# Kernel tuning notes

Hardware: AMD Instinct MI355X
Metric: run time of the kernel (lower is better)

The kernel has to match this reference:

```python
import jax, jax.numpy as jnp
import numpy as np

N_NODES = 100000
N_EDGES = 3200000
IN_CH = 16
HIDDEN = 32
NUM_HH = 1000


def setup_inputs() -> dict:
    key = jax.random.key(0)
    ks = jax.random.split(key, 10)
    x = jax.random.normal(ks[0], (N_NODES, IN_CH), dtype=jnp.float32)
    edge_index = jax.random.randint(ks[1], (2, N_EDGES), 0, N_NODES, dtype=jnp.int64)
    s = 1.0 / np.sqrt(IN_CH)
    w1_l = jax.random.uniform(ks[2], (IN_CH, HIDDEN), jnp.float32, -s, s)
    w1_r = jax.random.uniform(ks[3], (IN_CH, HIDDEN), jnp.float32, -s, s)
    b1 = jnp.zeros((HIDDEN,), jnp.float32)
    s2 = 1.0 / np.sqrt(HIDDEN)
    w2_l = jax.random.uniform(ks[4], (HIDDEN, HIDDEN), jnp.float32, -s2, s2)
    w2_r = jax.random.uniform(ks[5], (HIDDEN, HIDDEN), jnp.float32, -s2, s2)
    b2 = jnp.zeros((HIDDEN,), jnp.float32)
    fc_w = jax.random.uniform(ks[6], (HIDDEN, NUM_HH), jnp.float32, -s2, s2)
    fc_b = jnp.zeros((NUM_HH,), jnp.float32)
    return {"x": x, "edge_index": edge_index, "w1_l": w1_l, "w1_r": w1_r, "b1": b1,
            "w2_l": w2_l, "w2_r": w2_r, "b2": b2, "fc_w": fc_w, "fc_b": fc_b}


def _sage_conv(h, src, dst, w_l, w_r, b, n_nodes):
    # mean-aggregate source features onto targets (PyG SAGEConv, aggr='mean')
    msg = h[src]                                            # [E, F] gather
    agg = jax.ops.segment_sum(msg, dst, num_segments=n_nodes)
    cnt = jax.ops.segment_sum(jnp.ones((src.shape[0], 1), h.dtype), dst,
                              num_segments=n_nodes)
    mean = agg / jnp.maximum(cnt, 1.0)
    # out = lin_l(mean_neighbors) + lin_r(x); bias lives in lin_l
    return mean @ w_l + b + h @ w_r


def reference(x, edge_index, w1_l, w1_r, b1, w2_l, w2_r, b2, fc_w, fc_b):
    src, dst = edge_index[0], edge_index[1]
    n = x.shape[0]
    h = jax.nn.relu(_sage_conv(x, src, dst, w1_l, w1_r, b1, n))
    h = jax.nn.relu(_sage_conv(h, src, dst, w2_l, w2_r, b2, n))
    return h @ fc_w + fc_b
```

## Files before the change

### kernel.cpp

```cpp
#include <hip/hip_runtime.h>

#define N_NODES 100000
#define IN_CH 16
#define HIDDEN 32
#define NUM_HH 1000

#define NPB 128
#define NBUCK ((N_NODES + NPB - 1) / NPB)
#define NCHUNK 512
#define CAP 4480

__global__ __launch_bounds__(256) void passAB(
    const int* __restrict__ src, const int* __restrict__ dst,
    int* __restrict__ gcur, unsigned* __restrict__ packed, int n_edges,
    int cepb) {
  __shared__ int hist[NBUCK];
  __shared__ int rbase[NBUCK];
  __shared__ int cur[NBUCK];
  const int tid = threadIdx.x;
  for (int i = tid; i < NBUCK; i += 256) {
    hist[i] = 0;
    cur[i] = 0;
  }
  __syncthreads();

  const int s = blockIdx.x * cepb;
  const int e = min(n_edges, s + cepb);
  for (int i = s + tid; i < e; i += 256) atomicAdd(&hist[dst[i] >> 7], 1);
  __syncthreads();

  for (int b = tid; b < NBUCK; b += 256) {
    const int h = hist[b];
    rbase[b] = h ? atomicAdd(&gcur[b], h) : 0;
  }
  __syncthreads();

  for (int i = s + tid; i < e; i += 256) {
    const int d = dst[i];
    const int b = d >> 7;
    const int off = atomicAdd(&cur[b], 1);
    const int pos = rbase[b] + off;
    if (pos < CAP)
      packed[(size_t)b * CAP + pos] =
          (unsigned)src[i] | ((unsigned)(d & (NPB - 1)) << 17);
  }
}

__global__ __launch_bounds__(512) void bucket_sort(
    unsigned* __restrict__ packed, const int* __restrict__ gcur,
    int* __restrict__ row_ptr) {
  __shared__ unsigned stage[CAP];
  __shared__ int bins[NPB];
  __shared__ int scn[NPB];
  __shared__ int cur[NPB];
  const int b = blockIdx.x;
  const int base = b * CAP;
  const int cnt = min(gcur[b], CAP);
  const int tid = threadIdx.x;

  if (tid < NPB) bins[tid] = 0;
  __syncthreads();
  for (int i = tid; i < cnt; i += 512) {
    const unsigned pk = packed[base + i];
    stage[i] = pk;
    atomicAdd(&bins[pk >> 17], 1);
  }
  __syncthreads();
  if (tid < NPB) scn[tid] = bins[tid];
  __syncthreads();
  for (int off = 1; off < NPB; off <<= 1) {
    int t = (tid < NPB && tid >= off) ? scn[tid - off] : 0;
    __syncthreads();
    if (tid < NPB) scn[tid] += t;
    __syncthreads();
  }
  if (tid < NPB) {
    const int excl = scn[tid] - bins[tid];
    cur[tid] = excl;
    const int node = b * NPB + tid;
    if (node < N_NODES) row_ptr[node] = base + excl;
  }
  if (b == NBUCK - 1 && tid == 0) row_ptr[N_NODES] = base + cnt;
  __syncthreads();
  for (int i = tid; i < cnt; i += 512) {
    const unsigned pk = stage[i];
    const int pos = atomicAdd(&cur[pk >> 17], 1);
    packed[base + pos] = pk & 0x1FFFFu;
  }
}

template <int CH>
__global__ __launch_bounds__(512) void sage_block(
    const float* __restrict__ feat, const int* __restrict__ row_ptr,
    const unsigned* __restrict__ adj, const int* __restrict__ gcur,
    const float* __restrict__ w_l, const float* __restrict__ w_r,
    const float* __restrict__ b, float* __restrict__ out) {
  constexpr int Q = CH / 4;
  constexpr int EPW = 64 / Q;
  __shared__ unsigned s_adj[CAP];
  __shared__ float wl[CH * HIDDEN];
  __shared__ float wr[CH * HIDDEN];
  __shared__ float bs[HIDDEN];
  __shared__ float mean_s[8][CH];
  __shared__ float xs[8][CH];

  const int tid = threadIdx.x;
  const int bk = blockIdx.x;
  const int base = bk * NPB;
  const int bstart = bk * CAP;
  const int bcnt = min(gcur[bk], CAP);

  for (int i = tid; i < CH * HIDDEN; i += 512) {
    wl[i] = w_l[i];
    wr[i] = w_r[i];
  }
  if (tid < HIDDEN) bs[tid] = b[tid];
  for (int i = tid; i < bcnt; i += 512) s_adj[i] = adj[bstart + i];
  __syncthreads();

  const int wave = tid >> 6;
  const int lane = tid & 63;
  const int q = lane & (Q - 1);
  const int esub = lane / Q;
  const int j = lane & 31;
  const int p = lane >> 5;

#pragma unroll 1
  for (int pass = 0; pass < NPB / 8; ++pass) {
    const int l = pass * 8 + wave;
    const int n = base + l;
    if (n < N_NODES) {
      const int s = row_ptr[n] - bstart;
      const int e = (l == NPB - 1) ? bcnt : row_ptr[n + 1] - bstart;

      float4 xv = {0.f, 0.f, 0.f, 0.f};
      if (esub == 0) xv = ((const float4*)(feat + (size_t)n * CH))[q];

      float4 acc = {0.f, 0.f, 0.f, 0.f};
      for (int i = s + esub; i < e; i += EPW) {
        const int sn = (int)s_adj[i];
        const float4 v = ((const float4*)(feat + (size_t)sn * CH))[q];
        acc.x += v.x;
        acc.y += v.y;
        acc.z += v.z;
        acc.w += v.w;
      }
#pragma unroll
      for (int m = Q; m < 64; m <<= 1) {
        acc.x += __shfl_xor(acc.x, m, 64);
        acc.y += __shfl_xor(acc.y, m, 64);
        acc.z += __shfl_xor(acc.z, m, 64);
        acc.w += __shfl_xor(acc.w, m, 64);
      }
      const float inv = 1.0f / fmaxf((float)(e - s), 1.0f);
      if (esub == 0) {
        mean_s[wave][4 * q + 0] = acc.x * inv;
        mean_s[wave][4 * q + 1] = acc.y * inv;
        mean_s[wave][4 * q + 2] = acc.z * inv;
        mean_s[wave][4 * q + 3] = acc.w * inv;
        xs[wave][4 * q + 0] = xv.x;
        xs[wave][4 * q + 1] = xv.y;
        xs[wave][4 * q + 2] = xv.z;
        xs[wave][4 * q + 3] = xv.w;
      }
      __builtin_amdgcn_wave_barrier();

      float o = 0.f;
#pragma unroll
      for (int k = p * (CH / 2); k < (p + 1) * (CH / 2); ++k)
        o = fmaf(mean_s[wave][k], wl[k * HIDDEN + j],
                 fmaf(xs[wave][k], wr[k * HIDDEN + j], o));
      o += __shfl_xor(o, 32, 64);
      if (p == 0) out[(size_t)n * HIDDEN + j] = fmaxf(o + bs[j], 0.f);
      __builtin_amdgcn_wave_barrier();
    }
  }
}

#define FC_BN 128
__global__ __launch_bounds__(256) void fc_direct(
    const float* __restrict__ h, const float* __restrict__ fcw,
    const float* __restrict__ fcb, float* __restrict__ out) {
  const int tid = threadIdx.x;
  const int base = blockIdx.x * FC_BN;
  const int nvalid = min(FC_BN, N_NODES - base);

  float w[4][HIDDEN];
  float bias[4];
#pragma unroll
  for (int c = 0; c < 4; ++c) {
    const int j = c * 256 + tid;
    const bool valid = j < NUM_HH;
    bias[c] = valid ? fcb[j] : 0.f;
#pragma unroll
    for (int k = 0; k < HIDDEN; ++k)
      w[c][k] = valid ? fcw[k * NUM_HH + j] : 0.f;
  }

#pragma unroll 2
  for (int n = 0; n < nvalid; ++n) {
    const float4* hrow = (const float4*)(h + (size_t)(base + n) * HIDDEN);
    float a0 = bias[0], a1 = bias[1], a2 = bias[2], a3 = bias[3];
#pragma unroll
    for (int k4 = 0; k4 < HIDDEN / 4; ++k4) {
      const float4 hv = hrow[k4];
      a0 = fmaf(hv.x, w[0][4 * k4 + 0], a0);
      a0 = fmaf(hv.y, w[0][4 * k4 + 1], a0);
      a0 = fmaf(hv.z, w[0][4 * k4 + 2], a0);
      a0 = fmaf(hv.w, w[0][4 * k4 + 3], a0);
      a1 = fmaf(hv.x, w[1][4 * k4 + 0], a1);
      a1 = fmaf(hv.y, w[1][4 * k4 + 1], a1);
      a1 = fmaf(hv.z, w[1][4 * k4 + 2], a1);
      a1 = fmaf(hv.w, w[1][4 * k4 + 3], a1);
      a2 = fmaf(hv.x, w[2][4 * k4 + 0], a2);
      a2 = fmaf(hv.y, w[2][4 * k4 + 1], a2);
      a2 = fmaf(hv.z, w[2][4 * k4 + 2], a2);
      a2 = fmaf(hv.w, w[2][4 * k4 + 3], a2);
      a3 = fmaf(hv.x, w[3][4 * k4 + 0], a3);
      a3 = fmaf(hv.y, w[3][4 * k4 + 1], a3);
      a3 = fmaf(hv.z, w[3][4 * k4 + 2], a3);
      a3 = fmaf(hv.w, w[3][4 * k4 + 3], a3);
    }
    float* orow = out + (size_t)(base + n) * NUM_HH;
    orow[tid] = a0;
    orow[256 + tid] = a1;
    orow[512 + tid] = a2;
    if (768 + tid < NUM_HH) orow[768 + tid] = a3;
  }
}

extern "C" void kernel_launch(void* const* d_in, const int* in_sizes, int n_in,
                              void* d_out, int out_size, void* d_ws,
                              size_t ws_size, hipStream_t stream) {
  const float* x = (const float*)d_in[0];
  const int* edge = (const int*)d_in[1];
  const float* w1_l = (const float*)d_in[2];
  const float* w1_r = (const float*)d_in[3];
  const float* b1 = (const float*)d_in[4];
  const float* w2_l = (const float*)d_in[5];
  const float* w2_r = (const float*)d_in[6];
  const float* b2 = (const float*)d_in[7];
  const float* fc_w = (const float*)d_in[8];
  const float* fc_b = (const float*)d_in[9];
  float* out = (float*)d_out;

  const int n_edges = in_sizes[1] / 2;
  const int* src = edge;
  const int* dst = edge + n_edges;

  unsigned* packed = (unsigned*)d_ws;
  float* h1 = (float*)(packed + (size_t)NBUCK * CAP);
  float* h2 = h1 + (size_t)N_NODES * HIDDEN;
  int* gcur = (int*)(h2 + (size_t)N_NODES * HIDDEN);
  int* row_ptr = gcur + NBUCK;

  const int cepb = (n_edges + NCHUNK - 1) / NCHUNK;
  const int fgrid = (N_NODES + FC_BN - 1) / FC_BN;

  hipMemsetAsync(gcur, 0, NBUCK * sizeof(int), stream);
  passAB<<<NCHUNK, 256, 0, stream>>>(src, dst, gcur, packed, n_edges, cepb);
  bucket_sort<<<NBUCK, 512, 0, stream>>>(packed, gcur, row_ptr);

  sage_block<IN_CH><<<NBUCK, 512, 0, stream>>>(x, row_ptr, packed, gcur, w1_l,
                                               w1_r, b1, h1);
  sage_block<HIDDEN><<<NBUCK, 512, 0, stream>>>(h1, row_ptr, packed, gcur,
                                                w2_l, w2_r, b2, h2);
  fc_direct<<<fgrid, 256, 0, stream>>>(h2, fc_w, fc_b, out);
}
```

Baseline: 426.3 us.

## Fuse bucket sort into layer-1 SAGE and layer-2 SAGE into FC

The per-bucket sort is merged with the first SAGE layer, so the sorted adjacency stays in shared memory and per-node ranges come from the in-block scan instead of row_ptr. The second SAGE layer is merged with the final FC projection: h2 is kept in shared memory per 128-node bucket and multiplied by fc_w with 512 threads, each holding two output columns. This removes two launches and the h2 round-trip to global memory. In exchange, the FC stage now has only 782 blocks of 512 threads with heavy register use (64 weights per thread), and shared memory per block grows.

```diff
diff --git a/kernel.cpp b/kernel.cpp
--- a/kernel.cpp
+++ b/kernel.cpp
@@ -46,22 +46,41 @@
   }
 }
 
-__global__ __launch_bounds__(512) void bucket_sort(
+__global__ __launch_bounds__(512) void sort_sage1(
     unsigned* __restrict__ packed, const int* __restrict__ gcur,
-    int* __restrict__ row_ptr) {
+    int* __restrict__ row_ptr, const float* __restrict__ feat,
+    const float* __restrict__ w_l, const float* __restrict__ w_r,
+    const float* __restrict__ bias, float* __restrict__ out) {
+  constexpr int CH = IN_CH;
+  constexpr int Q = CH / 4;
+  constexpr int EPW = 64 / Q;
   __shared__ unsigned stage[CAP];
+  __shared__ unsigned s_adj[CAP];
   __shared__ int bins[NPB];
   __shared__ int scn[NPB];
   __shared__ int cur[NPB];
-  const int b = blockIdx.x;
-  const int base = b * CAP;
-  const int cnt = min(gcur[b], CAP);
+  __shared__ float wl[CH * HIDDEN];
+  __shared__ float wr[CH * HIDDEN];
+  __shared__ float bs[HIDDEN];
+  __shared__ float mean_s[8][CH];
+  __shared__ float xs[8][CH];
+
   const int tid = threadIdx.x;
-
+  const int bk = blockIdx.x;
+  const int base = bk * NPB;
+  const int gbase = bk * CAP;
+  const int cnt = min(gcur[bk], CAP);
+
+  for (int i = tid; i < CH * HIDDEN; i += 512) {
+    wl[i] = w_l[i];
+    wr[i] = w_r[i];
+  }
+  if (tid < HIDDEN) bs[tid] = bias[tid];
   if (tid < NPB) bins[tid] = 0;
   __syncthreads();
+
   for (int i = tid; i < cnt; i += 512) {
-    const unsigned pk = packed[base + i];
+    const unsigned pk = packed[gbase + i];
     stage[i] = pk;
     atomicAdd(&bins[pk >> 17], 1);
   }
@@ -77,46 +96,19 @@
   if (tid < NPB) {
     const int excl = scn[tid] - bins[tid];
     cur[tid] = excl;
-    const int node = b * NPB + tid;
-    if (node < N_NODES) row_ptr[node] = base + excl;
-  }
-  if (b == NBUCK - 1 && tid == 0) row_ptr[N_NODES] = base + cnt;
+    const int node = base + tid;
+    if (node < N_NODES) row_ptr[node] = gbase + excl;
+  }
+  if (bk == NBUCK - 1 && tid == 0) row_ptr[N_NODES] = gbase + cnt;
   __syncthreads();
   for (int i = tid; i < cnt; i += 512) {
     const unsigned pk = stage[i];
     const int pos = atomicAdd(&cur[pk >> 17], 1);
-    packed[base + pos] = pk & 0x1FFFFu;
-  }
-}
-
-template <int CH>
-__global__ __launch_bounds__(512) void sage_block(
-    const float* __restrict__ feat, const int* __restrict__ row_ptr,
-    const unsigned* __restrict__ adj, const int* __restrict__ gcur,
-    const float* __restrict__ w_l, const float* __restrict__ w_r,
-    const float* __restrict__ b, float* __restrict__ out) {
-  constexpr int Q = CH / 4;
-  constexpr int EPW = 64 / Q;
-  __shared__ unsigned s_adj[CAP];
-  __shared__ float wl[CH * HIDDEN];
-  __shared__ float wr[CH * HIDDEN];
-  __shared__ float bs[HIDDEN];
-  __shared__ float mean_s[8][CH];
-  __shared__ float xs[8][CH];
-
-  const int tid = threadIdx.x;
-  const int bk = blockIdx.x;
-  const int base = bk * NPB;
-  const int bstart = bk * CAP;
-  const int bcnt = min(gcur[bk], CAP);
-
-  for (int i = tid; i < CH * HIDDEN; i += 512) {
-    wl[i] = w_l[i];
-    wr[i] = w_r[i];
-  }
-  if (tid < HIDDEN) bs[tid] = b[tid];
-  for (int i = tid; i < bcnt; i += 512) s_adj[i] = adj[bstart + i];
-  __syncthreads();
+    s_adj[pos] = pk & 0x1FFFFu;
+  }
+  __syncthreads();
+
+  for (int i = tid; i < cnt; i += 512) packed[gbase + i] = s_adj[i];
 
   const int wave = tid >> 6;
   const int lane = tid & 63;
@@ -130,8 +122,8 @@
     const int l = pass * 8 + wave;
     const int n = base + l;
     if (n < N_NODES) {
-      const int s = row_ptr[n] - bstart;
-      const int e = (l == NPB - 1) ? bcnt : row_ptr[n + 1] - bstart;
+      const int s = scn[l] - bins[l];
+      const int e = scn[l];
 
       float4 xv = {0.f, 0.f, 0.f, 0.f};
       if (esub == 0) xv = ((const float4*)(feat + (size_t)n * CH))[q];
@@ -177,55 +169,130 @@
   }
 }
 
-#define FC_BN 128
-__global__ __launch_bounds__(256) void fc_direct(
-    const float* __restrict__ h, const float* __restrict__ fcw,
+__global__ __launch_bounds__(512, 4) void sage2_fc(
+    const float* __restrict__ feat, const int* __restrict__ row_ptr,
+    const unsigned* __restrict__ adj, const int* __restrict__ gcur,
+    const float* __restrict__ w_l, const float* __restrict__ w_r,
+    const float* __restrict__ bias, const float* __restrict__ fcw,
     const float* __restrict__ fcb, float* __restrict__ out) {
+  constexpr int CH = HIDDEN;
+  constexpr int Q = CH / 4;
+  constexpr int EPW = 64 / Q;
+  __shared__ unsigned s_adj[CAP];
+  __shared__ float wl[CH * HIDDEN];
+  __shared__ float wr[CH * HIDDEN];
+  __shared__ float bs[HIDDEN];
+  __shared__ float mean_s[8][CH];
+  __shared__ float xs[8][CH];
+  __shared__ float hs[NPB * HIDDEN];
+
   const int tid = threadIdx.x;
-  const int base = blockIdx.x * FC_BN;
-  const int nvalid = min(FC_BN, N_NODES - base);
-
-  float w[4][HIDDEN];
-  float bias[4];
-#pragma unroll
-  for (int c = 0; c < 4; ++c) {
-    const int j = c * 256 + tid;
-    const bool valid = j < NUM_HH;
-    bias[c] = valid ? fcb[j] : 0.f;
-#pragma unroll
-    for (int k = 0; k < HIDDEN; ++k)
-      w[c][k] = valid ? fcw[k * NUM_HH + j] : 0.f;
+  const int bk = blockIdx.x;
+  const int base = bk * NPB;
+  const int gbase = bk * CAP;
+  const int bcnt = min(gcur[bk], CAP);
+
+  for (int i = tid; i < CH * HIDDEN; i += 512) {
+    wl[i] = w_l[i];
+    wr[i] = w_r[i];
+  }
+  if (tid < HIDDEN) bs[tid] = bias[tid];
+  for (int i = tid; i < bcnt; i += 512) s_adj[i] = adj[gbase + i];
+  __syncthreads();
+
+  const int wave = tid >> 6;
+  const int lane = tid & 63;
+  const int q = lane & (Q - 1);
+  const int esub = lane / Q;
+  const int j = lane & 31;
+  const int p = lane >> 5;
+
+#pragma unroll 1
+  for (int pass = 0; pass < NPB / 8; ++pass) {
+    const int l = pass * 8 + wave;
+    const int n = base + l;
+    if (n < N_NODES) {
+      const int s = row_ptr[n] - gbase;
+      const int e = (l == NPB - 1) ? bcnt : row_ptr[n + 1] - gbase;
+
+      float4 xv = {0.f, 0.f, 0.f, 0.f};
+      if (esub == 0) xv = ((const float4*)(feat + (size_t)n * CH))[q];
+
+      float4 acc = {0.f, 0.f, 0.f, 0.f};
+      for (int i = s + esub; i < e; i += EPW) {
+        const int sn = (int)s_adj[i];
+        const float4 v = ((const float4*)(feat + (size_t)sn * CH))[q];
+        acc.x += v.x;
+        acc.y += v.y;
+        acc.z += v.z;
+        acc.w += v.w;
+      }
+#pragma unroll
+      for (int m = Q; m < 64; m <<= 1) {
+        acc.x += __shfl_xor(acc.x, m, 64);
+        acc.y += __shfl_xor(acc.y, m, 64);
+        acc.z += __shfl_xor(acc.z, m, 64);
+        acc.w += __shfl_xor(acc.w, m, 64);
+      }
+      const float inv = 1.0f / fmaxf((float)(e - s), 1.0f);
+      if (esub == 0) {
+        mean_s[wave][4 * q + 0] = acc.x * inv;
+        mean_s[wave][4 * q + 1] = acc.y * inv;
+        mean_s[wave][4 * q + 2] = acc.z * inv;
+        mean_s[wave][4 * q + 3] = acc.w * inv;
+        xs[wave][4 * q + 0] = xv.x;
+        xs[wave][4 * q + 1] = xv.y;
+        xs[wave][4 * q + 2] = xv.z;
+        xs[wave][4 * q + 3] = xv.w;
+      }
+      __builtin_amdgcn_wave_barrier();
+
+      float o = 0.f;
+#pragma unroll
+      for (int k = p * (CH / 2); k < (p + 1) * (CH / 2); ++k)
+        o = fmaf(mean_s[wave][k], wl[k * HIDDEN + j],
+                 fmaf(xs[wave][k], wr[k * HIDDEN + j], o));
+      o += __shfl_xor(o, 32, 64);
+      if (p == 0) hs[l * HIDDEN + j] = fmaxf(o + bs[j], 0.f);
+      __builtin_amdgcn_wave_barrier();
+    }
+  }
+  __syncthreads();
+
+  const int nvalid = min(NPB, N_NODES - base);
+  float w0[HIDDEN], w1[HIDDEN];
+  float bb0, bb1;
+  {
+    const int j0 = tid;
+    const int j1 = 512 + tid;
+    bb0 = fcb[j0];
+    bb1 = (j1 < NUM_HH) ? fcb[j1] : 0.f;
+#pragma unroll
+    for (int k = 0; k < HIDDEN; ++k) {
+      w0[k] = fcw[k * NUM_HH + j0];
+      w1[k] = (j1 < NUM_HH) ? fcw[k * NUM_HH + j1] : 0.f;
+    }
   }
 
 #pragma unroll 2
   for (int n = 0; n < nvalid; ++n) {
-    const float4* hrow = (const float4*)(h + (size_t)(base + n) * HIDDEN);
-    float a0 = bias[0], a1 = bias[1], a2 = bias[2], a3 = bias[3];
+    const float4* hrow = (const float4*)(hs + n * HIDDEN);
+    float a0 = bb0, a1 = bb1;
 #pragma unroll
     for (int k4 = 0; k4 < HIDDEN / 4; ++k4) {
       const float4 hv = hrow[k4];
-      a0 = fmaf(hv.x, w[0][4 * k4 + 0], a0);
-      a0 = fmaf(hv.y, w[0][4 * k4 + 1], a0);
-      a0 = fmaf(hv.z, w[0][4 * k4 + 2], a0);
-      a0 = fmaf(hv.w, w[0][4 * k4 + 3], a0);
-      a1 = fmaf(hv.x, w[1][4 * k4 + 0], a1);
-      a1 = fmaf(hv.y, w[1][4 * k4 + 1], a1);
-      a1 = fmaf(hv.z, w[1][4 * k4 + 2], a1);
-      a1 = fmaf(hv.w, w[1][4 * k4 + 3], a1);
-      a2 = fmaf(hv.x, w[2][4 * k4 + 0], a2);
-      a2 = fmaf(hv.y, w[2][4 * k4 + 1], a2);
-      a2 = fmaf(hv.z, w[2][4 * k4 + 2], a2);
-      a2 = fmaf(hv.w, w[2][4 * k4 + 3], a2);
-      a3 = fmaf(hv.x, w[3][4 * k4 + 0], a3);
-      a3 = fmaf(hv.y, w[3][4 * k4 + 1], a3);
-      a3 = fmaf(hv.z, w[3][4 * k4 + 2], a3);
-      a3 = fmaf(hv.w, w[3][4 * k4 + 3], a3);
+      a0 = fmaf(hv.x, w0[4 * k4 + 0], a0);
+      a0 = fmaf(hv.y, w0[4 * k4 + 1], a0);
+      a0 = fmaf(hv.z, w0[4 * k4 + 2], a0);
+      a0 = fmaf(hv.w, w0[4 * k4 + 3], a0);
+      a1 = fmaf(hv.x, w1[4 * k4 + 0], a1);
+      a1 = fmaf(hv.y, w1[4 * k4 + 1], a1);
+      a1 = fmaf(hv.z, w1[4 * k4 + 2], a1);
+      a1 = fmaf(hv.w, w1[4 * k4 + 3], a1);
     }
     float* orow = out + (size_t)(base + n) * NUM_HH;
     orow[tid] = a0;
-    orow[256 + tid] = a1;
-    orow[512 + tid] = a2;
-    if (768 + tid < NUM_HH) orow[768 + tid] = a3;
+    if (512 + tid < NUM_HH) orow[512 + tid] = a1;
   }
 }
 
@@ -250,20 +317,17 @@
 
   unsigned* packed = (unsigned*)d_ws;
   float* h1 = (float*)(packed + (size_t)NBUCK * CAP);
-  float* h2 = h1 + (size_t)N_NODES * HIDDEN;
-  int* gcur = (int*)(h2 + (size_t)N_NODES * HIDDEN);
+  int* gcur = (int*)(h1 + (size_t)N_NODES * HIDDEN);
   int* row_ptr = gcur + NBUCK;
 
   const int cepb = (n_edges + NCHUNK - 1) / NCHUNK;
-  const int fgrid = (N_NODES + FC_BN - 1) / FC_BN;
 
   hipMemsetAsync(gcur, 0, NBUCK * sizeof(int), stream);
   passAB<<<NCHUNK, 256, 0, stream>>>(src, dst, gcur, packed, n_edges, cepb);
-  bucket_sort<<<NBUCK, 512, 0, stream>>>(packed, gcur, row_ptr);
-
-  sage_block<IN_CH><<<NBUCK, 512, 0, stream>>>(x, row_ptr, packed, gcur, w1_l,
-                                               w1_r, b1, h1);
-  sage_block<HIDDEN><<<NBUCK, 512, 0, stream>>>(h1, row_ptr, packed, gcur,
-                                                w2_l, w2_r, b2, h2);
-  fc_direct<<<fgrid, 256, 0, stream>>>(h2, fc_w, fc_b, out);
+
+  sort_sage1<<<NBUCK, 512, 0, stream>>>(packed, gcur, row_ptr, x, w1_l, w1_r,
+                                        b1, h1);
+
+  sage2_fc<<<NBUCK, 512, 0, stream>>>(h1, row_ptr, packed, gcur, w2_l, w2_r,
+                                      b2, fc_w, fc_b, out);
 }
```

New measurement: 1.065 ms. 2.5x slower.

## Fuse bucket sort into first SAGE layer and store hidden features as fp16

Applied to the files above, without the earlier changes.

Merges the per-bucket sort kernel with the first SAGEConv layer, so the sorted adjacency stays in shared memory and the row bounds come from the in-block scan instead of a global reload. The first layer's output is now written as half precision, and the second layer gathers 16-byte fp16 rows, halving the bytes moved per neighbour gather. This saves one launch and one adjacency round trip but adds fp16 rounding of the intermediate activations and raises shared memory use in the fused kernel.

```diff
diff --git a/kernel.cpp b/kernel.cpp
--- a/kernel.cpp
+++ b/kernel.cpp
@@ -1,4 +1,5 @@
 #include <hip/hip_runtime.h>
+#include <hip/hip_fp16.h>
 
 #define N_NODES 100000
 #define IN_CH 16
@@ -46,22 +47,41 @@
   }
 }
 
-__global__ __launch_bounds__(512) void bucket_sort(
+__global__ __launch_bounds__(512) void sort_sage1(
     unsigned* __restrict__ packed, const int* __restrict__ gcur,
-    int* __restrict__ row_ptr) {
+    int* __restrict__ row_ptr, const float* __restrict__ feat,
+    const float* __restrict__ w_l, const float* __restrict__ w_r,
+    const float* __restrict__ bias, __half* __restrict__ out) {
+  constexpr int CH = IN_CH;
+  constexpr int Q = CH / 4;
+  constexpr int EPW = 64 / Q;
   __shared__ unsigned stage[CAP];
+  __shared__ unsigned s_adj[CAP];
   __shared__ int bins[NPB];
   __shared__ int scn[NPB];
   __shared__ int cur[NPB];
-  const int b = blockIdx.x;
-  const int base = b * CAP;
-  const int cnt = min(gcur[b], CAP);
+  __shared__ float wl[CH * HIDDEN];
+  __shared__ float wr[CH * HIDDEN];
+  __shared__ float bs[HIDDEN];
+  __shared__ float mean_s[8][CH];
+  __shared__ float xs[8][CH];
+
   const int tid = threadIdx.x;
-
+  const int bk = blockIdx.x;
+  const int base = bk * NPB;
+  const int gbase = bk * CAP;
+  const int cnt = min(gcur[bk], CAP);
+
+  for (int i = tid; i < CH * HIDDEN; i += 512) {
+    wl[i] = w_l[i];
+    wr[i] = w_r[i];
+  }
+  if (tid < HIDDEN) bs[tid] = bias[tid];
   if (tid < NPB) bins[tid] = 0;
   __syncthreads();
+
   for (int i = tid; i < cnt; i += 512) {
-    const unsigned pk = packed[base + i];
+    const unsigned pk = packed[gbase + i];
     stage[i] = pk;
     atomicAdd(&bins[pk >> 17], 1);
   }
@@ -77,46 +97,19 @@
   if (tid < NPB) {
     const int excl = scn[tid] - bins[tid];
     cur[tid] = excl;
-    const int node = b * NPB + tid;
-    if (node < N_NODES) row_ptr[node] = base + excl;
-  }
-  if (b == NBUCK - 1 && tid == 0) row_ptr[N_NODES] = base + cnt;
+    const int node = base + tid;
+    if (node < N_NODES) row_ptr[node] = gbase + excl;
+  }
+  if (bk == NBUCK - 1 && tid == 0) row_ptr[N_NODES] = gbase + cnt;
   __syncthreads();
   for (int i = tid; i < cnt; i += 512) {
     const unsigned pk = stage[i];
     const int pos = atomicAdd(&cur[pk >> 17], 1);
-    packed[base + pos] = pk & 0x1FFFFu;
-  }
-}
-
-template <int CH>
-__global__ __launch_bounds__(512) void sage_block(
-    const float* __restrict__ feat, const int* __restrict__ row_ptr,
-    const unsigned* __restrict__ adj, const int* __restrict__ gcur,
-    const float* __restrict__ w_l, const float* __restrict__ w_r,
-    const float* __restrict__ b, float* __restrict__ out) {
-  constexpr int Q = CH / 4;
-  constexpr int EPW = 64 / Q;
-  __shared__ unsigned s_adj[CAP];
-  __shared__ float wl[CH * HIDDEN];
-  __shared__ float wr[CH * HIDDEN];
-  __shared__ float bs[HIDDEN];
-  __shared__ float mean_s[8][CH];
-  __shared__ float xs[8][CH];
-
-  const int tid = threadIdx.x;
-  const int bk = blockIdx.x;
-  const int base = bk * NPB;
-  const int bstart = bk * CAP;
-  const int bcnt = min(gcur[bk], CAP);
-
-  for (int i = tid; i < CH * HIDDEN; i += 512) {
-    wl[i] = w_l[i];
-    wr[i] = w_r[i];
-  }
-  if (tid < HIDDEN) bs[tid] = b[tid];
-  for (int i = tid; i < bcnt; i += 512) s_adj[i] = adj[bstart + i];
-  __syncthreads();
+    s_adj[pos] = pk & 0x1FFFFu;
+  }
+  __syncthreads();
+
+  for (int i = tid; i < cnt; i += 512) packed[gbase + i] = s_adj[i];
 
   const int wave = tid >> 6;
   const int lane = tid & 63;
@@ -130,8 +123,8 @@
     const int l = pass * 8 + wave;
     const int n = base + l;
     if (n < N_NODES) {
-      const int s = row_ptr[n] - bstart;
-      const int e = (l == NPB - 1) ? bcnt : row_ptr[n + 1] - bstart;
+      const int s = scn[l] - bins[l];
+      const int e = scn[l];
 
       float4 xv = {0.f, 0.f, 0.f, 0.f};
       if (esub == 0) xv = ((const float4*)(feat + (size_t)n * CH))[q];
@@ -162,6 +155,103 @@
         xs[wave][4 * q + 1] = xv.y;
         xs[wave][4 * q + 2] = xv.z;
         xs[wave][4 * q + 3] = xv.w;
+      }
+      __builtin_amdgcn_wave_barrier();
+
+      float o = 0.f;
+#pragma unroll
+      for (int k = p * (CH / 2); k < (p + 1) * (CH / 2); ++k)
+        o = fmaf(mean_s[wave][k], wl[k * HIDDEN + j],
+                 fmaf(xs[wave][k], wr[k * HIDDEN + j], o));
+      o += __shfl_xor(o, 32, 64);
+      if (p == 0) out[(size_t)n * HIDDEN + j] = __float2half(fmaxf(o + bs[j], 0.f));
+      __builtin_amdgcn_wave_barrier();
+    }
+  }
+}
+
+__global__ __launch_bounds__(512) void sage2(
+    const __half* __restrict__ feat, const int* __restrict__ row_ptr,
+    const unsigned* __restrict__ adj, const int* __restrict__ gcur,
+    const float* __restrict__ w_l, const float* __restrict__ w_r,
+    const float* __restrict__ bias, float* __restrict__ out) {
+  constexpr int CH = HIDDEN;
+  constexpr int Q = 4;
+  constexpr int EPW = 16;
+  __shared__ unsigned s_adj[CAP];
+  __shared__ float wl[CH * HIDDEN];
+  __shared__ float wr[CH * HIDDEN];
+  __shared__ float bs[HIDDEN];
+  __shared__ float mean_s[8][CH];
+  __shared__ float xs[8][CH];
+
+  const int tid = threadIdx.x;
+  const int bk = blockIdx.x;
+  const int base = bk * NPB;
+  const int gbase = bk * CAP;
+  const int bcnt = min(gcur[bk], CAP);
+
+  for (int i = tid; i < CH * HIDDEN; i += 512) {
+    wl[i] = w_l[i];
+    wr[i] = w_r[i];
+  }
+  if (tid < HIDDEN) bs[tid] = bias[tid];
+  for (int i = tid; i < bcnt; i += 512) s_adj[i] = adj[gbase + i];
+  __syncthreads();
+
+  const int wave = tid >> 6;
+  const int lane = tid & 63;
+  const int q = lane & 3;
+  const int esub = lane >> 2;
+  const int j = lane & 31;
+  const int p = lane >> 5;
+
+#pragma unroll 1
+  for (int pass = 0; pass < NPB / 8; ++pass) {
+    const int l = pass * 8 + wave;
+    const int n = base + l;
+    if (n < N_NODES) {
+      const int s = row_ptr[n] - gbase;
+      const int e = (l == NPB - 1) ? bcnt : row_ptr[n + 1] - gbase;
+
+      uint4 xu = {0, 0, 0, 0};
+      if (esub == 0) xu = ((const uint4*)(feat + (size_t)n * CH))[q];
+
+      float acc[8] = {0.f, 0.f, 0.f, 0.f, 0.f, 0.f, 0.f, 0.f};
+      for (int i = s + esub; i < e; i += EPW) {
+        const int sn = (int)s_adj[i];
+        union {
+          uint4 u;
+          __half2 h[4];
+        } U;
+        U.u = ((const uint4*)(feat + (size_t)sn * CH))[q];
+#pragma unroll
+        for (int t = 0; t < 4; ++t) {
+          const float2 f = __half22float2(U.h[t]);
+          acc[2 * t] += f.x;
+          acc[2 * t + 1] += f.y;
+        }
+      }
+#pragma unroll
+      for (int m = Q; m < 64; m <<= 1) {
+#pragma unroll
+        for (int t = 0; t < 8; ++t) acc[t] += __shfl_xor(acc[t], m, 64);
+      }
+      const float inv = 1.0f / fmaxf((float)(e - s), 1.0f);
+      if (esub == 0) {
+#pragma unroll
+        for (int t = 0; t < 8; ++t) mean_s[wave][8 * q + t] = acc[t] * inv;
+        union {
+          uint4 u;
+          __half2 h[4];
+        } X;
+        X.u = xu;
+#pragma unroll
+        for (int t = 0; t < 4; ++t) {
+          const float2 f = __half22float2(X.h[t]);
+          xs[wave][8 * q + 2 * t] = f.x;
+          xs[wave][8 * q + 2 * t + 1] = f.y;
+        }
       }
       __builtin_amdgcn_wave_barrier();
 
@@ -249,8 +339,8 @@
   const int* dst = edge + n_edges;
 
   unsigned* packed = (unsigned*)d_ws;
-  float* h1 = (float*)(packed + (size_t)NBUCK * CAP);
-  float* h2 = h1 + (size_t)N_NODES * HIDDEN;
+  __half* h1 = (__half*)(packed + (size_t)NBUCK * CAP);
+  float* h2 = (float*)(h1 + (size_t)N_NODES * HIDDEN);
   int* gcur = (int*)(h2 + (size_t)N_NODES * HIDDEN);
   int* row_ptr = gcur + NBUCK;
 
@@ -259,11 +349,12 @@
 
   hipMemsetAsync(gcur, 0, NBUCK * sizeof(int), stream);
   passAB<<<NCHUNK, 256, 0, stream>>>(src, dst, gcur, packed, n_edges, cepb);
-  bucket_sort<<<NBUCK, 512, 0, stream>>>(packed, gcur, row_ptr);
-
-  sage_block<IN_CH><<<NBUCK, 512, 0, stream>>>(x, row_ptr, packed, gcur, w1_l,
-                                               w1_r, b1, h1);
-  sage_block<HIDDEN><<<NBUCK, 512, 0, stream>>>(h1, row_ptr, packed, gcur,
-                                                w2_l, w2_r, b2, h2);
+
+  sort_sage1<<<NBUCK, 512, 0, stream>>>(packed, gcur, row_ptr, x, w1_l, w1_r,
+                                        b1, h1);
+
+  sage2<<<NBUCK, 512, 0, stream>>>(h1, row_ptr, packed, gcur, w2_l, w2_r, b2,
+                                   h2);
+
   fc_direct<<<fgrid, 256, 0, stream>>>(h2, fc_w, fc_b, out);
 }
```

Result: no change. 419.4 us (-1.6%).
